# Performance work log

Hardware: AMD Instinct MI355X
Metric: run time of the kernel (lower is better)

Reference implementation:

```python
import jax, jax.numpy as jnp
import numpy as np

INPUT_DIM = 256
N_NODES = 100000
N_EDGES = 500000


def setup_inputs() -> dict:
    key = jax.random.key(0)
    ks = jax.random.split(key, 10)
    d = INPUT_DIM

    def linear(kw, kb, fan_in, fan_out):
        # torch nn.Linear default init: U(-1/sqrt(fan_in), 1/sqrt(fan_in))
        bound = 1.0 / np.sqrt(fan_in)
        W = jax.random.uniform(kw, (fan_out, fan_in), jnp.float32, -bound, bound)
        b = jax.random.uniform(kb, (fan_out,), jnp.float32, -bound, bound)
        return W, b

    W1, b1 = linear(ks[0], ks[1], 2 * d, 2 * d)
    W2, b2 = linear(ks[2], ks[3], 2 * d, d)
    W3, b3 = linear(ks[4], ks[5], d, d)
    W4, b4 = linear(ks[6], ks[7], d, 1)

    z = jax.random.normal(ks[8], (N_NODES, d), jnp.float32)
    edge_index = jax.random.randint(ks[9], (2, N_EDGES), 0, N_NODES, jnp.int64)
    return {
        "z": z, "edge_index": edge_index,
        "W1": W1, "b1": b1, "W2": W2, "b2": b2,
        "W3": W3, "b3": b3, "W4": W4, "b4": b4,
    }


def reference(z, edge_index, W1, b1, W2, b2, W3, b3, W4, b4):
    row, col = edge_index[0], edge_index[1]
    # gather endpoint embeddings and concat: [E, 2d]
    z_concat = jnp.concatenate([z[row], z[col]], axis=1)
    # dropout is identity in eval mode (reference runs deterministic)
    x = jax.nn.relu(z_concat @ W1.T + b1)
    x = jax.nn.relu(x @ W2.T + b2)
    x = jax.nn.relu(x @ W3.T + b3)
    return jax.nn.sigmoid(x @ W4.T + b4)  # [E, 1]
```

## Files before the change

kernel.cpp:

```cpp
#include <hip/hip_runtime.h>
#include <math.h>


typedef _Float16 f16x8 __attribute__((ext_vector_type(8)));
typedef _Float16 f16x4 __attribute__((ext_vector_type(4)));
typedef float    f32x4 __attribute__((ext_vector_type(4)));

#define W1E (512*512)
#define W2E (256*512)
#define W3E (256*256)
#define WTOT (W1E+W2E+W3E)
#define H_OFF 1048576

__global__ void repack_w(const float* __restrict__ W1, const float* __restrict__ W2,
                         const float* __restrict__ W3, _Float16* __restrict__ wout) {
  int t = blockIdx.x * 256 + threadIdx.x;
  if (t >= WTOT) return;
  const float* src; _Float16* dst; int K, idx;
  if (t < W1E)            { src = W1; K = 512; idx = t;             dst = wout; }
  else if (t < W1E + W2E) { src = W2; K = 512; idx = t - W1E;       dst = wout + W1E; }
  else                    { src = W3; K = 256; idx = t - (W1E+W2E); dst = wout + W1E + W2E; }
  int j    = idx & 7;
  int lane = (idx >> 3) & 63;
  int rest = idx >> 9;
  int ktiles = K >> 5;
  int kt = rest % ktiles;
  int nt = rest / ktiles;
  int n = nt * 16 + (lane & 15);
  int k = kt * 32 + (lane >> 4) * 8 + j;
  dst[idx] = (_Float16)src[n * K + k];
}

__global__ __launch_bounds__(512, 2)
void precompute_h2(const float* __restrict__ z, int N, const float* __restrict__ b1,
                   const _Float16* __restrict__ w1, _Float16* __restrict__ H) {
  __shared__ char smem[32768];
  const int tid  = threadIdx.x;
  const int wid  = tid >> 6;
  const int lane = tid & 63;
  const int l15  = lane & 15;
  const int lhi  = lane >> 4;
  const int nbase = blockIdx.x * 64;
  const int half = wid >> 2;
  const int wloc = wid & 3;

  for (int r = wid; r < 64; r += 8) {
    int n = nbase + r; if (n >= N) n = N - 1;
    float4 v = *(const float4*)(z + (size_t)n * 256 + lane * 4);
    f16x4 h;
    h[0] = (_Float16)v.x; h[1] = (_Float16)v.y; h[2] = (_Float16)v.z; h[3] = (_Float16)v.w;
    *(f16x4*)(smem + r * 512 + ((lane * 8) ^ ((r & 7) << 4))) = h;
  }
  __syncthreads();

  for (int p = 0; p < 2; ++p) {
    f32x4 acc[4][4];
    #pragma unroll
    for (int nt = 0; nt < 4; ++nt) {
      f32x4 bv = (f32x4){0.f, 0.f, 0.f, 0.f};
      if (half == 0) bv = *(const f32x4*)(b1 + wloc*128 + p*64 + nt*16 + lhi*4);
      #pragma unroll
      for (int et = 0; et < 4; ++et) acc[nt][et] = bv;
    }

    for (int kt = 0; kt < 8; ++kt) {
      int ktg = kt + half * 8;
      f16x8 wf[4], xf[4];
      #pragma unroll
      for (int nt = 0; nt < 4; ++nt) {
        int ntg = wloc*8 + p*4 + nt;
        wf[nt] = *(const f16x8*)(w1 + (((ntg*16 + ktg)*64 + lane)) * 8);
      }
      #pragma unroll
      for (int et = 0; et < 4; ++et) {
        int r = et*16 + l15;
        xf[et] = *(const f16x8*)(smem + r * 512 + ((kt*64 + lhi*16) ^ ((r & 7) << 4)));
      }
      #pragma unroll
      for (int nt = 0; nt < 4; ++nt)
        #pragma unroll
        for (int et = 0; et < 4; ++et)
          acc[nt][et] = __builtin_amdgcn_mfma_f32_16x16x32_f16(wf[nt], xf[et], acc[nt][et], 0, 0, 0);
    }

    #pragma unroll
    for (int nt = 0; nt < 4; ++nt)
      #pragma unroll
      for (int et = 0; et < 4; ++et) {
        int n = nbase + et*16 + l15;
        if (n < N) {
          f16x4 h;
          #pragma unroll
          for (int r = 0; r < 4; ++r) h[r] = (_Float16)acc[nt][et][r];
          *(f16x4*)(H + (size_t)n * 1024 + half*512 + wloc*128 + p*64 + nt*16 + lhi*4) = h;
        }
      }
  }
}

#define SCR_OFF  24576
#define LDS2_BYTES 49152

__global__ __launch_bounds__(512, 6)
void fused_edges48(const int* __restrict__ ei, int E, const _Float16* __restrict__ H,
                   const float* __restrict__ b2, const float* __restrict__ b3,
                   const float* __restrict__ W4, const float* __restrict__ b4,
                   const _Float16* __restrict__ w2, const _Float16* __restrict__ w3,
                   float* __restrict__ out) {
  extern __shared__ char smem[];
  float* scr = (float*)(smem + SCR_OFF);

  const int tid  = threadIdx.x;
  const int wid  = tid >> 6;
  const int lane = tid & 63;
  const int l15  = lane & 15;
  const int lhi  = lane >> 4;
  const int base = blockIdx.x * 48;

  #pragma unroll 3
  for (int e = wid; e < 48; e += 8) {
    int ge = base + e; if (ge >= E) ge = E - 1;
    int nr = ei[ge];
    int nc = ei[E + ge];
    f16x8 ha = *(const f16x8*)(H + (size_t)nr * 1024 + lane * 8);
    f16x8 hb = *(const f16x8*)(H + (size_t)nc * 1024 + 512 + lane * 8);
    f16x8 s = ha + hb;
    #pragma unroll
    for (int j = 0; j < 8; ++j) s[j] = (s[j] > (_Float16)0) ? s[j] : (_Float16)0;
    *(f16x8*)(smem + e * 1024 + ((lane * 16) ^ ((e & 7) << 4))) = s;
  }
  __syncthreads();

  f32x4 acc2[2][3];
  #pragma unroll
  for (int nt = 0; nt < 2; ++nt) {
    f32x4 bv = *(const f32x4*)(b2 + wid*32 + nt*16 + lhi*4);
    #pragma unroll
    for (int et = 0; et < 3; ++et) acc2[nt][et] = bv;
  }
  for (int kt = 0; kt < 16; ++kt) {
    f16x8 wf[2], xf[3];
    #pragma unroll
    for (int nt = 0; nt < 2; ++nt)
      wf[nt] = *(const f16x8*)(w2 + (((wid*2 + nt)*16 + kt)*64 + lane) * 8);
    #pragma unroll
    for (int et = 0; et < 3; ++et) {
      int e = et*16 + l15;
      xf[et] = *(const f16x8*)(smem + e * 1024 + ((kt*64 + lhi*16) ^ ((e & 7) << 4)));
    }
    #pragma unroll
    for (int nt = 0; nt < 2; ++nt)
      #pragma unroll
      for (int et = 0; et < 3; ++et)
        acc2[nt][et] = __builtin_amdgcn_mfma_f32_16x16x32_f16(wf[nt], xf[et], acc2[nt][et], 0, 0, 0);
  }
  __syncthreads();
  #pragma unroll
  for (int nt = 0; nt < 2; ++nt)
    #pragma unroll
    for (int et = 0; et < 3; ++et) {
      int e = et*16 + l15;
      int ncb = (wid*32 + nt*16 + lhi*4) * 2;
      f16x4 h;
      #pragma unroll
      for (int r = 0; r < 4; ++r) h[r] = (_Float16)fmaxf(acc2[nt][et][r], 0.f);
      *(f16x4*)(smem + e * 512 + (ncb ^ ((e & 7) << 4))) = h;
    }
  __syncthreads();

  f32x4 acc3[2][3];
  #pragma unroll
  for (int nt = 0; nt < 2; ++nt) {
    f32x4 bv = *(const f32x4*)(b3 + wid*32 + nt*16 + lhi*4);
    #pragma unroll
    for (int et = 0; et < 3; ++et) acc3[nt][et] = bv;
  }
  for (int kt = 0; kt < 8; ++kt) {
    f16x8 wf[2], xf[3];
    #pragma unroll
    for (int nt = 0; nt < 2; ++nt)
      wf[nt] = *(const f16x8*)(w3 + (((wid*2 + nt)*8 + kt)*64 + lane) * 8);
    #pragma unroll
    for (int et = 0; et < 3; ++et) {
      int e = et*16 + l15;
      xf[et] = *(const f16x8*)(smem + e * 512 + ((kt*64 + lhi*16) ^ ((e & 7) << 4)));
    }
    #pragma unroll
    for (int nt = 0; nt < 2; ++nt)
      #pragma unroll
      for (int et = 0; et < 3; ++et)
        acc3[nt][et] = __builtin_amdgcn_mfma_f32_16x16x32_f16(wf[nt], xf[et], acc3[nt][et], 0, 0, 0);
  }

  f32x4 w4v[2];
  #pragma unroll
  for (int nt = 0; nt < 2; ++nt)
    w4v[nt] = *(const f32x4*)(W4 + wid*32 + nt*16 + lhi*4);

  #pragma unroll
  for (int et = 0; et < 3; ++et) {
    float p = 0.f;
    #pragma unroll
    for (int nt = 0; nt < 2; ++nt)
      #pragma unroll
      for (int r = 0; r < 4; ++r)
        p += fmaxf(acc3[nt][et][r], 0.f) * w4v[nt][r];
    p += __shfl_xor(p, 16);
    p += __shfl_xor(p, 32);
    if (lane < 16) scr[(et*16 + l15) * 8 + wid] = p;
  }
  __syncthreads();

  if (tid < 48) {
    int ge = base + tid;
    if (ge < E) {
      float s = b4[0];
      #pragma unroll
      for (int w = 0; w < 8; ++w) s += scr[tid*8 + w];
      out[ge] = 1.f / (1.f + expf(-s));
    }
  }
}

#define FSCR_OFF  65536
#define FBIAS_OFF 67584
#define FLDS_BYTES 72832

__global__ __launch_bounds__(512, 2)
void fused_fallback(const float* __restrict__ z, const int* __restrict__ ei, int E,
                    const float* __restrict__ b1, const float* __restrict__ b2,
                    const float* __restrict__ b3, const float* __restrict__ W4,
                    const float* __restrict__ b4,
                    const _Float16* __restrict__ wbuf, float* __restrict__ out) {
  extern __shared__ char smem[];
  float* scr = (float*)(smem + FSCR_OFF);
  float* bls = (float*)(smem + FBIAS_OFF);

  const int tid  = threadIdx.x;
  const int wid  = tid >> 6;
  const int lane = tid & 63;
  const int l15  = lane & 15;
  const int lhi  = lane >> 4;
  const int base = blockIdx.x * 64;

  for (int i = tid; i < 1281; i += 512) {
    float v;
    if (i < 512)       v = b1[i];
    else if (i < 768)  v = b2[i - 512];
    else if (i < 1024) v = b3[i - 768];
    else if (i < 1280) v = W4[i - 1024];
    else               v = b4[0];
    bls[i] = v;
  }

  for (int it = wid; it < 128; it += 8) {
    int e = it >> 1, hf = it & 1;
    int ge = base + e; if (ge >= E) ge = E - 1;
    int src = ei[hf ? (E + ge) : ge];
    float4 v = *(const float4*)(z + (size_t)src * 256 + lane * 4);
    f16x4 h;
    h[0] = (_Float16)v.x; h[1] = (_Float16)v.y; h[2] = (_Float16)v.z; h[3] = (_Float16)v.w;
    *(f16x4*)(smem + e * 1024 + ((hf * 512 + lane * 8) ^ ((e & 7) << 4))) = h;
  }
  __syncthreads();

  const _Float16* w1 = wbuf;
  const _Float16* w2 = wbuf + W1E;
  const _Float16* w3 = wbuf + W1E + W2E;

  f32x4 acc1[4][4];
  #pragma unroll
  for (int nt = 0; nt < 4; ++nt) {
    f32x4 bv = *(const f32x4*)(bls + wid*64 + nt*16 + lhi*4);
    #pragma unroll
    for (int et = 0; et < 4; ++et) acc1[nt][et] = bv;
  }
  for (int kt = 0; kt < 16; ++kt) {
    f16x8 wf[4], xf[4];
    #pragma unroll
    for (int nt = 0; nt < 4; ++nt)
      wf[nt] = *(const f16x8*)(w1 + (((wid*4 + nt)*16 + kt)*64 + lane) * 8);
    #pragma unroll
    for (int et = 0; et < 4; ++et) {
      int e = et*16 + l15;
      xf[et] = *(const f16x8*)(smem + e * 1024 + ((kt*64 + lhi*16) ^ ((e & 7) << 4)));
    }
    #pragma unroll
    for (int nt = 0; nt < 4; ++nt)
      #pragma unroll
      for (int et = 0; et < 4; ++et)
        acc1[nt][et] = __builtin_amdgcn_mfma_f32_16x16x32_f16(wf[nt], xf[et], acc1[nt][et], 0, 0, 0);
  }
  __syncthreads();
  #pragma unroll
  for (int nt = 0; nt < 4; ++nt)
    #pragma unroll
    for (int et = 0; et < 4; ++et) {
      int e = et*16 + l15;
      int ncb = (wid*64 + nt*16 + lhi*4) * 2;
      f16x4 h;
      #pragma unroll
      for (int r = 0; r < 4; ++r) h[r] = (_Float16)fmaxf(acc1[nt][et][r], 0.f);
      *(f16x4*)(smem + e * 1024 + (ncb ^ ((e & 7) << 4))) = h;
    }
  __syncthreads();

  f32x4 acc2[2][4];
  #pragma unroll
  for (int nt = 0; nt < 2; ++nt) {
    f32x4 bv = *(const f32x4*)(bls + 512 + wid*32 + nt*16 + lhi*4);
    #pragma unroll
    for (int et = 0; et < 4; ++et) acc2[nt][et] = bv;
  }
  for (int kt = 0; kt < 16; ++kt) {
    f16x8 wf[2], xf[4];
    #pragma unroll
    for (int nt = 0; nt < 2; ++nt)
      wf[nt] = *(const f16x8*)(w2 + (((wid*2 + nt)*16 + kt)*64 + lane) * 8);
    #pragma unroll
    for (int et = 0; et < 4; ++et) {
      int e = et*16 + l15;
      xf[et] = *(const f16x8*)(smem + e * 1024 + ((kt*64 + lhi*16) ^ ((e & 7) << 4)));
    }
    #pragma unroll
    for (int nt = 0; nt < 2; ++nt)
      #pragma unroll
      for (int et = 0; et < 4; ++et)
        acc2[nt][et] = __builtin_amdgcn_mfma_f32_16x16x32_f16(wf[nt], xf[et], acc2[nt][et], 0, 0, 0);
  }
  __syncthreads();
  #pragma unroll
  for (int nt = 0; nt < 2; ++nt)
    #pragma unroll
    for (int et = 0; et < 4; ++et) {
      int e = et*16 + l15;
      int ncb = (wid*32 + nt*16 + lhi*4) * 2;
      f16x4 h;
      #pragma unroll
      for (int r = 0; r < 4; ++r) h[r] = (_Float16)fmaxf(acc2[nt][et][r], 0.f);
      *(f16x4*)(smem + e * 512 + (ncb ^ ((e & 7) << 4))) = h;
    }
  __syncthreads();

  f32x4 acc3[2][4];
  #pragma unroll
  for (int nt = 0; nt < 2; ++nt) {
    f32x4 bv = *(const f32x4*)(bls + 768 + wid*32 + nt*16 + lhi*4);
    #pragma unroll
    for (int et = 0; et < 4; ++et) acc3[nt][et] = bv;
  }
  for (int kt = 0; kt < 8; ++kt) {
    f16x8 wf[2], xf[4];
    #pragma unroll
    for (int nt = 0; nt < 2; ++nt)
      wf[nt] = *(const f16x8*)(w3 + (((wid*2 + nt)*8 + kt)*64 + lane) * 8);
    #pragma unroll
    for (int et = 0; et < 4; ++et) {
      int e = et*16 + l15;
      xf[et] = *(const f16x8*)(smem + e * 512 + ((kt*64 + lhi*16) ^ ((e & 7) << 4)));
    }
    #pragma unroll
    for (int nt = 0; nt < 2; ++nt)
      #pragma unroll
      for (int et = 0; et < 4; ++et)
        acc3[nt][et] = __builtin_amdgcn_mfma_f32_16x16x32_f16(wf[nt], xf[et], acc3[nt][et], 0, 0, 0);
  }

  f32x4 w4v[2];
  #pragma unroll
  for (int nt = 0; nt < 2; ++nt)
    w4v[nt] = *(const f32x4*)(bls + 1024 + wid*32 + nt*16 + lhi*4);
  float bias4 = bls[1280];

  #pragma unroll
  for (int et = 0; et < 4; ++et) {
    float p = 0.f;
    #pragma unroll
    for (int nt = 0; nt < 2; ++nt)
      #pragma unroll
      for (int r = 0; r < 4; ++r)
        p += fmaxf(acc3[nt][et][r], 0.f) * w4v[nt][r];
    p += __shfl_xor(p, 16);
    p += __shfl_xor(p, 32);
    if (lane < 16) scr[(et*16 + l15) * 8 + wid] = p;
  }
  __syncthreads();

  if (tid < 64) {
    int ge = base + tid;
    if (ge < E) {
      float s = bias4;
      #pragma unroll
      for (int w = 0; w < 8; ++w) s += scr[tid*8 + w];
      out[ge] = 1.f / (1.f + expf(-s));
    }
  }
}

extern "C" void kernel_launch(void* const* d_in, const int* in_sizes, int n_in,
                              void* d_out, int out_size, void* d_ws, size_t ws_size,
                              hipStream_t stream) {
  const float* z  = (const float*)d_in[0];
  const int*   ei = (const int*)d_in[1];
  const float* W1 = (const float*)d_in[2];
  const float* b1 = (const float*)d_in[3];
  const float* W2 = (const float*)d_in[4];
  const float* b2 = (const float*)d_in[5];
  const float* W3 = (const float*)d_in[6];
  const float* b3 = (const float*)d_in[7];
  const float* W4 = (const float*)d_in[8];
  const float* b4 = (const float*)d_in[9];
  float* out = (float*)d_out;
  const int E = in_sizes[1] / 2;
  const int N = in_sizes[0] / 256;

  _Float16* wbuf = (_Float16*)d_ws;
  _Float16* H    = (_Float16*)((char*)d_ws + H_OFF);

  repack_w<<<(WTOT + 255) / 256, 256, 0, stream>>>(W1, W2, W3, wbuf);

  size_t need = (size_t)H_OFF + (size_t)N * 1024 * 2;
  if (ws_size >= need) {
    precompute_h2<<<(N + 63) / 64, 512, 0, stream>>>(z, N, b1, wbuf, H);
    int nblk = (E + 47) / 48;
    fused_edges48<<<nblk, 512, LDS2_BYTES, stream>>>(ei, E, H, b2, b3, W4, b4,
                                                     wbuf + W1E, wbuf + W1E + W2E, out);
  } else {
    int nblk = (E + 63) / 64;
    fused_fallback<<<nblk, 512, FLDS_BYTES, stream>>>(z, ei, E, b1, b2, b3, W4, b4, wbuf, out);
  }
}
```

Baseline: 416.8 us.

## Retile node precompute and edge MLP kernels with 2x4 warp grid over 64 edges

The node precompute kernel is rewritten as precompute_h3: 256-thread blocks over 32 nodes, each warp computing a 2x2 MFMA tile across eight passes, aiming for more resident blocks per CU. The edge kernel now handles 64 edges per block with warps arranged 2 (edge rows) by 4 (output columns). Each warp loads four weight fragments per two activation fragments, which raises weight reuse per MFMA and reduces redundant global weight loads. In exchange the edge kernel needs about 65 KB of LDS and launch bounds of 2, down from 6, so fewer edge blocks can be resident to hide the random gather latency.

```diff
diff --git a/kernel.cpp b/kernel.cpp
--- a/kernel.cpp
+++ b/kernel.cpp
@@ -31,20 +31,20 @@
   dst[idx] = (_Float16)src[n * K + k];
 }
 
-__global__ __launch_bounds__(512, 2)
-void precompute_h2(const float* __restrict__ z, int N, const float* __restrict__ b1,
+__global__ __launch_bounds__(256, 6)
+void precompute_h3(const float* __restrict__ z, int N, const float* __restrict__ b1,
                    const _Float16* __restrict__ w1, _Float16* __restrict__ H) {
-  __shared__ char smem[32768];
+  __shared__ char smem[16384];
   const int tid  = threadIdx.x;
   const int wid  = tid >> 6;
   const int lane = tid & 63;
   const int l15  = lane & 15;
   const int lhi  = lane >> 4;
-  const int nbase = blockIdx.x * 64;
-  const int half = wid >> 2;
-  const int wloc = wid & 3;
-
-  for (int r = wid; r < 64; r += 8) {
+  const int nbase = blockIdx.x * 32;
+  const int half = wid >> 1;
+  const int col  = wid & 1;
+
+  for (int r = wid; r < 32; r += 4) {
     int n = nbase + r; if (n >= N) n = N - 1;
     float4 v = *(const float4*)(z + (size_t)n * 256 + lane * 4);
     f16x4 h;
@@ -53,72 +53,76 @@
   }
   __syncthreads();
 
-  for (int p = 0; p < 2; ++p) {
-    f32x4 acc[4][4];
-    #pragma unroll
-    for (int nt = 0; nt < 4; ++nt) {
+  for (int pass = 0; pass < 8; ++pass) {
+    f32x4 acc[2][2];
+    #pragma unroll
+    for (int nt = 0; nt < 2; ++nt) {
       f32x4 bv = (f32x4){0.f, 0.f, 0.f, 0.f};
-      if (half == 0) bv = *(const f32x4*)(b1 + wloc*128 + p*64 + nt*16 + lhi*4);
-      #pragma unroll
-      for (int et = 0; et < 4; ++et) acc[nt][et] = bv;
+      if (half == 0) bv = *(const f32x4*)(b1 + col*256 + pass*32 + nt*16 + lhi*4);
+      #pragma unroll
+      for (int et = 0; et < 2; ++et) acc[nt][et] = bv;
     }
 
     for (int kt = 0; kt < 8; ++kt) {
       int ktg = kt + half * 8;
-      f16x8 wf[4], xf[4];
-      #pragma unroll
-      for (int nt = 0; nt < 4; ++nt) {
-        int ntg = wloc*8 + p*4 + nt;
-        wf[nt] = *(const f16x8*)(w1 + (((ntg*16 + ktg)*64 + lane)) * 8);
+      f16x8 wf[2], xf[2];
+      #pragma unroll
+      for (int nt = 0; nt < 2; ++nt) {
+        int ntg = col*16 + pass*2 + nt;
+        wf[nt] = *(const f16x8*)(w1 + ((ntg*16 + ktg)*64 + lane) * 8);
       }
       #pragma unroll
-      for (int et = 0; et < 4; ++et) {
+      for (int et = 0; et < 2; ++et) {
         int r = et*16 + l15;
         xf[et] = *(const f16x8*)(smem + r * 512 + ((kt*64 + lhi*16) ^ ((r & 7) << 4)));
       }
       #pragma unroll
-      for (int nt = 0; nt < 4; ++nt)
+      for (int nt = 0; nt < 2; ++nt)
         #pragma unroll
-        for (int et = 0; et < 4; ++et)
+        for (int et = 0; et < 2; ++et)
           acc[nt][et] = __builtin_amdgcn_mfma_f32_16x16x32_f16(wf[nt], xf[et], acc[nt][et], 0, 0, 0);
     }
 
     #pragma unroll
-    for (int nt = 0; nt < 4; ++nt)
-      #pragma unroll
-      for (int et = 0; et < 4; ++et) {
-        int n = nbase + et*16 + l15;
-        if (n < N) {
+    for (int et = 0; et < 2; ++et)
+      #pragma unroll
+      for (int nt = 0; nt < 2; ++nt) {
+        int gn = nbase + et*16 + l15;
+        if (gn < N) {
           f16x4 h;
           #pragma unroll
           for (int r = 0; r < 4; ++r) h[r] = (_Float16)acc[nt][et][r];
-          *(f16x4*)(H + (size_t)n * 1024 + half*512 + wloc*128 + p*64 + nt*16 + lhi*4) = h;
+          *(f16x4*)(H + (size_t)gn*1024 + wid*256 + pass*32 + nt*16 + lhi*4) = h;
         }
       }
   }
 }
 
-#define SCR_OFF  24576
-#define LDS2_BYTES 49152
-
-__global__ __launch_bounds__(512, 6)
-void fused_edges48(const int* __restrict__ ei, int E, const _Float16* __restrict__ H,
+#define SCR64_OFF 65536
+#define LDS64_BYTES 66560
+
+__global__ __launch_bounds__(512, 2)
+void fused_edges64(const int* __restrict__ ei, int E,
+                   const _Float16* __restrict__ H,
                    const float* __restrict__ b2, const float* __restrict__ b3,
                    const float* __restrict__ W4, const float* __restrict__ b4,
                    const _Float16* __restrict__ w2, const _Float16* __restrict__ w3,
                    float* __restrict__ out) {
   extern __shared__ char smem[];
-  float* scr = (float*)(smem + SCR_OFF);
+  float* scr = (float*)(smem + SCR64_OFF);
 
   const int tid  = threadIdx.x;
   const int wid  = tid >> 6;
   const int lane = tid & 63;
   const int l15  = lane & 15;
   const int lhi  = lane >> 4;
-  const int base = blockIdx.x * 48;
-
-  #pragma unroll 3
-  for (int e = wid; e < 48; e += 8) {
+  const int wr   = wid >> 2;
+  const int wc   = wid & 3;
+  const int base = blockIdx.x * 64;
+
+  #pragma unroll 4
+  for (int i = 0; i < 8; ++i) {
+    int e = i*8 + wid;
     int ge = base + e; if (ge >= E) ge = E - 1;
     int nr = ei[ge];
     int nc = ei[E + ge];
@@ -131,36 +135,36 @@
   }
   __syncthreads();
 
-  f32x4 acc2[2][3];
-  #pragma unroll
-  for (int nt = 0; nt < 2; ++nt) {
-    f32x4 bv = *(const f32x4*)(b2 + wid*32 + nt*16 + lhi*4);
-    #pragma unroll
-    for (int et = 0; et < 3; ++et) acc2[nt][et] = bv;
+  f32x4 acc2[4][2];
+  #pragma unroll
+  for (int nt = 0; nt < 4; ++nt) {
+    f32x4 bv = *(const f32x4*)(b2 + wc*64 + nt*16 + lhi*4);
+    #pragma unroll
+    for (int et = 0; et < 2; ++et) acc2[nt][et] = bv;
   }
   for (int kt = 0; kt < 16; ++kt) {
-    f16x8 wf[2], xf[3];
-    #pragma unroll
-    for (int nt = 0; nt < 2; ++nt)
-      wf[nt] = *(const f16x8*)(w2 + (((wid*2 + nt)*16 + kt)*64 + lane) * 8);
-    #pragma unroll
-    for (int et = 0; et < 3; ++et) {
-      int e = et*16 + l15;
+    f16x8 wf[4], xf[2];
+    #pragma unroll
+    for (int nt = 0; nt < 4; ++nt)
+      wf[nt] = *(const f16x8*)(w2 + (((wc*4 + nt)*16 + kt)*64 + lane) * 8);
+    #pragma unroll
+    for (int et = 0; et < 2; ++et) {
+      int e = wr*32 + et*16 + l15;
       xf[et] = *(const f16x8*)(smem + e * 1024 + ((kt*64 + lhi*16) ^ ((e & 7) << 4)));
     }
     #pragma unroll
-    for (int nt = 0; nt < 2; ++nt)
-      #pragma unroll
-      for (int et = 0; et < 3; ++et)
+    for (int nt = 0; nt < 4; ++nt)
+      #pragma unroll
+      for (int et = 0; et < 2; ++et)
         acc2[nt][et] = __builtin_amdgcn_mfma_f32_16x16x32_f16(wf[nt], xf[et], acc2[nt][et], 0, 0, 0);
   }
   __syncthreads();
   #pragma unroll
-  for (int nt = 0; nt < 2; ++nt)
-    #pragma unroll
-    for (int et = 0; et < 3; ++et) {
-      int e = et*16 + l15;
-      int ncb = (wid*32 + nt*16 + lhi*4) * 2;
+  for (int nt = 0; nt < 4; ++nt)
+    #pragma unroll
+    for (int et = 0; et < 2; ++et) {
+      int e = wr*32 + et*16 + l15;
+      int ncb = (wc*64 + nt*16 + lhi*4) * 2;
       f16x4 h;
       #pragma unroll
       for (int r = 0; r < 4; ++r) h[r] = (_Float16)fmaxf(acc2[nt][et][r], 0.f);
@@ -168,55 +172,53 @@
     }
   __syncthreads();
 
-  f32x4 acc3[2][3];
-  #pragma unroll
-  for (int nt = 0; nt < 2; ++nt) {
-    f32x4 bv = *(const f32x4*)(b3 + wid*32 + nt*16 + lhi*4);
-    #pragma unroll
-    for (int et = 0; et < 3; ++et) acc3[nt][et] = bv;
+  f32x4 acc3[4][2];
+  #pragma unroll
+  for (int nt = 0; nt < 4; ++nt) {
+    f32x4 bv = *(const f32x4*)(b3 + wc*64 + nt*16 + lhi*4);
+    #pragma unroll
+    for (int et = 0; et < 2; ++et) acc3[nt][et] = bv;
   }
   for (int kt = 0; kt < 8; ++kt) {
-    f16x8 wf[2], xf[3];
-    #pragma unroll
-    for (int nt = 0; nt < 2; ++nt)
-      wf[nt] = *(const f16x8*)(w3 + (((wid*2 + nt)*8 + kt)*64 + lane) * 8);
-    #pragma unroll
-    for (int et = 0; et < 3; ++et) {
-      int e = et*16 + l15;
+    f16x8 wf[4], xf[2];
+    #pragma unroll
+    for (int nt = 0; nt < 4; ++nt)
+      wf[nt] = *(const f16x8*)(w3 + (((wc*4 + nt)*8 + kt)*64 + lane) * 8);
+    #pragma unroll
+    for (int et = 0; et < 2; ++et) {
+      int e = wr*32 + et*16 + l15;
       xf[et] = *(const f16x8*)(smem + e * 512 + ((kt*64 + lhi*16) ^ ((e & 7) << 4)));
     }
     #pragma unroll
-    for (int nt = 0; nt < 2; ++nt)
-      #pragma unroll
-      for (int et = 0; et < 3; ++et)
+    for (int nt = 0; nt < 4; ++nt)
+      #pragma unroll
+      for (int et = 0; et < 2; ++et)
         acc3[nt][et] = __builtin_amdgcn_mfma_f32_16x16x32_f16(wf[nt], xf[et], acc3[nt][et], 0, 0, 0);
   }
 
-  f32x4 w4v[2];
-  #pragma unroll
-  for (int nt = 0; nt < 2; ++nt)
-    w4v[nt] = *(const f32x4*)(W4 + wid*32 + nt*16 + lhi*4);
-
-  #pragma unroll
-  for (int et = 0; et < 3; ++et) {
+  f32x4 w4v[4];
+  #pragma unroll
+  for (int nt = 0; nt < 4; ++nt)
+    w4v[nt] = *(const f32x4*)(W4 + wc*64 + nt*16 + lhi*4);
+
+  #pragma unroll
+  for (int et = 0; et < 2; ++et) {
     float p = 0.f;
     #pragma unroll
-    for (int nt = 0; nt < 2; ++nt)
+    for (int nt = 0; nt < 4; ++nt)
       #pragma unroll
       for (int r = 0; r < 4; ++r)
         p += fmaxf(acc3[nt][et][r], 0.f) * w4v[nt][r];
     p += __shfl_xor(p, 16);
     p += __shfl_xor(p, 32);
-    if (lane < 16) scr[(et*16 + l15) * 8 + wid] = p;
-  }
-  __syncthreads();
-
-  if (tid < 48) {
+    if (lane < 16) scr[(wr*32 + et*16 + l15) * 4 + wc] = p;
+  }
+  __syncthreads();
+
+  if (tid < 64) {
     int ge = base + tid;
     if (ge < E) {
-      float s = b4[0];
-      #pragma unroll
-      for (int w = 0; w < 8; ++w) s += scr[tid*8 + w];
+      float s = b4[0] + scr[tid*4+0] + scr[tid*4+1] + scr[tid*4+2] + scr[tid*4+3];
       out[ge] = 1.f / (1.f + expf(-s));
     }
   }
@@ -421,10 +423,10 @@
 
   size_t need = (size_t)H_OFF + (size_t)N * 1024 * 2;
   if (ws_size >= need) {
-    precompute_h2<<<(N + 63) / 64, 512, 0, stream>>>(z, N, b1, wbuf, H);
-    int nblk = (E + 47) / 48;
-    fused_edges48<<<nblk, 512, LDS2_BYTES, stream>>>(ei, E, H, b2, b3, W4, b4,
-                                                     wbuf + W1E, wbuf + W1E + W2E, out);
+    precompute_h3<<<(N + 31) / 32, 256, 0, stream>>>(z, N, b1, wbuf, H);
+    int nblk = (E + 63) / 64;
+    fused_edges64<<<nblk, 512, LDS64_BYTES, stream>>>(ei, E, H, b2, b3, W4, b4,
+                                                      wbuf + W1E, wbuf + W1E + W2E, out);
   } else {
     int nblk = (E + 63) / 64;
     fused_fallback<<<nblk, 512, FLDS_BYTES, stream>>>(z, ei, E, b1, b2, b3, W4, b4, wbuf, out);
```

Measured after the change: 809.1 us. +94.1%, slower.
